# Kernel optimization log

Hardware: AMD Instinct MI355X
Metric: run time of the kernel (lower is better)

Reference implementation:

```python
import jax, jax.numpy as jnp
import numpy as np

B, H, W, C, NC = 4, 64, 64, 64, 19


def setup_inputs() -> dict:
    key = jax.random.key(0)
    ks = jax.random.split(key, 12)
    s = 0.05  # small init so sigmoid scores are not saturated
    return {
        "feature": jax.random.normal(ks[0], (B, H, W, C), dtype=jnp.float32),
        "predict": jax.random.normal(ks[1], (B, H, W, NC), dtype=jnp.float32),
        # height attention params (dim = H); k_linear in source is unused (q reused as k)
        "hq_w": jax.random.normal(ks[2], (H, H), dtype=jnp.float32) * s,
        "hq_b": jnp.zeros((H,), dtype=jnp.float32),
        "hv_w": jax.random.normal(ks[3], (H, H), dtype=jnp.float32) * s,
        "hv_b": jnp.zeros((H,), dtype=jnp.float32),
        # width attention params (dim = W)
        "wq_w": jax.random.normal(ks[4], (W, W), dtype=jnp.float32) * s,
        "wq_b": jnp.zeros((W,), dtype=jnp.float32),
        "wv_w": jax.random.normal(ks[5], (W, W), dtype=jnp.float32) * s,
        "wv_b": jnp.zeros((W,), dtype=jnp.float32),
        # gating scalars (nn.Parameter(torch.zeros(1)) in source; random here to exercise path)
        "h_gate": jax.random.normal(ks[6], (1,), dtype=jnp.float32) * 0.5,
        "w_gate": jax.random.normal(ks[7], (1,), dtype=jnp.float32) * 0.5,
        # 1x1 conv num_classes -> 1 (stored as [NC, 1] matrix; 1x1 conv == per-pixel linear)
        "conv_w": jax.random.normal(ks[8], (NC, 1), dtype=jnp.float32) * s,
        "conv_b": jnp.zeros((1,), dtype=jnp.float32),
    }


def _self_atten(x, wq, bq, wv, bv, dim):
    # Source uses q_linear for BOTH q and k (k_linear dead), softmax replaced by sigmoid.
    q = x @ wq + bq                                   # [B, N, dim]
    v = x @ wv + bv                                   # [B, N, dim]
    scores = jax.nn.sigmoid(jnp.einsum('bnd,bmd->bnm', q, q) / jnp.sqrt(jnp.float32(dim)))
    return jnp.einsum('bnm,bmd->bnd', scores, v)      # [B, N, dim]


def _axial(x, hq_w, hq_b, hv_w, hv_b, wq_w, wq_b, wv_w, wv_b, h_gate, w_gate):
    b, h, w, c = x.shape
    # height attention: seq = W*C, feature dim = H
    xh = x.transpose(0, 2, 3, 1).reshape(b, w * c, h)
    xh = _self_atten(xh, hq_w, hq_b, hv_w, hv_b, h)
    xh = xh.reshape(b, w, c, h).transpose(0, 3, 1, 2)  # back to [B,H,W,C]
    x = xh * h_gate + x
    # width attention: seq = H*C, feature dim = W
    xw = x.transpose(0, 1, 3, 2).reshape(b, h * c, w)
    xw = _self_atten(xw, wq_w, wq_b, wv_w, wv_b, w)
    xw = xw.reshape(b, h, c, w).transpose(0, 1, 3, 2)  # back to [B,H,W,C]
    x = xw * w_gate + x
    return x


def reference(feature, predict, hq_w, hq_b, hv_w, hv_b, wq_w, wq_b, wv_w, wv_b,
              h_gate, w_gate, conv_w, conv_b):
    feat = feature + _axial(feature, hq_w, hq_b, hv_w, hv_b,
                            wq_w, wq_b, wv_w, wv_b, h_gate, w_gate)
    p = 1.0 - jax.nn.sigmoid(predict)                 # [B,H,W,NC]
    p = p @ conv_w + conv_b                           # 1x1 conv -> [B,H,W,1]
    return p * feat                                   # broadcast gate -> [B,H,W,C]
```

## Files before the change

### kernel.cpp

```cpp
#include <hip/hip_runtime.h>

typedef _Float16 f16x8 __attribute__((ext_vector_type(8)));
typedef __fp16   fp16x2 __attribute__((ext_vector_type(2)));
typedef float f32x16 __attribute__((ext_vector_type(16)));

__device__ __forceinline__ unsigned pkrtz(float a, float b) {
    fp16x2 h = __builtin_amdgcn_cvt_pkrtz(a, b);
    union { fp16x2 h; unsigned u; } c; c.h = h; return c.u;
}

__device__ __forceinline__ unsigned short f2h(float f) {
    _Float16 h = (_Float16)f;
    union { _Float16 h; unsigned short s; } c; c.h = h; return c.s;
}

__global__ __launch_bounds__(256) void prep_kernel(
    const float* __restrict__ src,
    const float* __restrict__ wq, const float* __restrict__ bq,
    const float* __restrict__ wv, const float* __restrict__ bv,
    unsigned short* __restrict__ Qg, unsigned short* __restrict__ Vtg)
{
    __shared__ float slab[64][65];
    __shared__ float wqs[4096];
    __shared__ float wvs[4096];

    const int t  = threadIdx.x;
    const int bx = blockIdx.x, b = blockIdx.y;

    {
        const float4* wq4 = (const float4*)wq;
        const float4* wv4 = (const float4*)wv;
        float4* q4 = (float4*)wqs; float4* v4 = (float4*)wvs;
        #pragma unroll
        for (int i = 0; i < 4; ++i) {
            q4[i*256 + t] = wq4[i*256 + t];
            v4[i*256 + t] = wv4[i*256 + t];
        }
    }
    {
        const int k = t >> 2, c0 = (t & 3) << 4;
        const size_t sb = (size_t)b*262144 + (size_t)k*4096 + (size_t)bx*64 + c0;
        #pragma unroll
        for (int i = 0; i < 4; ++i)
            *(float4*)&slab[k][c0 + i*4] = *(const float4*)&src[sb + i*4];
    }
    __syncthreads();

    const int c = t & 63, jg = t >> 6;
    float qa[16], va[16];
    #pragma unroll
    for (int jj = 0; jj < 16; ++jj) { qa[jj] = bq[jg*16+jj]; va[jj] = bv[jg*16+jj]; }
    for (int k = 0; k < 64; ++k) {
        const float xv = slab[k][c];
        const float* wqr = &wqs[k*64 + jg*16];
        const float* wvr = &wvs[k*64 + jg*16];
        #pragma unroll
        for (int jj = 0; jj < 16; ++jj) {
            qa[jj] += xv * wqr[jj];
            va[jj] += xv * wvr[jj];
        }
    }
    const int token = bx*64 + c;
    union { unsigned u[8]; uint4 v[2]; } qp;
    #pragma unroll
    for (int jj = 0; jj < 8; ++jj) qp.u[jj] = pkrtz(qa[2*jj], qa[2*jj+1]);
    const size_t qoff = ((size_t)b*4096 + token)*64 + jg*16;
    *(uint4*)&Qg[qoff]     = qp.v[0];
    *(uint4*)&Qg[qoff + 8] = qp.v[1];
    #pragma unroll
    for (int jj = 0; jj < 16; ++jj)
        Vtg[((size_t)b*64 + jg*16 + jj)*4096 + token] = f2h(va[jj]);
}

__global__ __launch_bounds__(256) void prep_w_kernel(
    const float* __restrict__ feature, const float* __restrict__ Pin,
    const float* __restrict__ gate,
    const float* __restrict__ wq, const float* __restrict__ bq,
    const float* __restrict__ wv, const float* __restrict__ bv,
    unsigned short* __restrict__ Qg, unsigned short* __restrict__ Vtg,
    float* __restrict__ x1out, int nsplit)
{
    __shared__ float slab[64][65];
    __shared__ float wqs[4096];
    __shared__ float wvs[4096];

    const int t  = threadIdx.x;
    const int bx = blockIdx.x, b = blockIdx.y;

    {
        const float4* wq4 = (const float4*)wq;
        const float4* wv4 = (const float4*)wv;
        float4* q4 = (float4*)wqs; float4* v4 = (float4*)wvs;
        #pragma unroll
        for (int i = 0; i < 4; ++i) {
            q4[i*256 + t] = wq4[i*256 + t];
            v4[i*256 + t] = wv4[i*256 + t];
        }
    }
    {
        const int k = t >> 2, c0 = (t & 3) << 4;
        const size_t off = (size_t)bx*4096 + (size_t)k*64 + c0;
        const size_t fb  = (size_t)b*262144 + off;
        const float g = gate[0];
        #pragma unroll
        for (int i = 0; i < 4; ++i) {
            float4 v  = *(const float4*)&feature[fb + i*4];
            float sx = 0.f, sy = 0.f, sz = 0.f, sw = 0.f;
            for (int ks = 0; ks < nsplit; ++ks) {
                float4 pk = *(const float4*)&Pin[((size_t)(ks*4 + b) << 18) + off + i*4];
                sx += pk.x; sy += pk.y; sz += pk.z; sw += pk.w;
            }
            v.x += g * sx; v.y += g * sy; v.z += g * sz; v.w += g * sw;
            *(float4*)&slab[k][c0 + i*4] = v;
            *(float4*)&x1out[fb + i*4] = v;
        }
    }
    __syncthreads();

    const int c = t & 63, jg = t >> 6;
    float qa[16], va[16];
    #pragma unroll
    for (int jj = 0; jj < 16; ++jj) { qa[jj] = bq[jg*16+jj]; va[jj] = bv[jg*16+jj]; }
    for (int k = 0; k < 64; ++k) {
        const float xv = slab[k][c];
        const float* wqr = &wqs[k*64 + jg*16];
        const float* wvr = &wvs[k*64 + jg*16];
        #pragma unroll
        for (int jj = 0; jj < 16; ++jj) {
            qa[jj] += xv * wqr[jj];
            va[jj] += xv * wvr[jj];
        }
    }
    const int token = bx*64 + c;
    union { unsigned u[8]; uint4 v[2]; } qp;
    #pragma unroll
    for (int jj = 0; jj < 8; ++jj) qp.u[jj] = pkrtz(qa[2*jj], qa[2*jj+1]);
    const size_t qoff = ((size_t)b*4096 + token)*64 + jg*16;
    *(uint4*)&Qg[qoff]     = qp.v[0];
    *(uint4*)&Qg[qoff + 8] = qp.v[1];
    #pragma unroll
    for (int jj = 0; jj < 16; ++jj)
        Vtg[((size_t)b*64 + jg*16 + jj)*4096 + token] = f2h(va[jj]);
}

__global__ __launch_bounds__(256) void attn_kernel(
    const unsigned short* __restrict__ Qg,
    const unsigned short* __restrict__ Vtg,
    float* __restrict__ P)
{
    __shared__ unsigned short Ksh[2][64][72];
    __shared__ unsigned short Vts[2][64][72];

    const int t = threadIdx.x;
    const int mb = blockIdx.x, b = blockIdx.y, ksplit = blockIdx.z;
    const int nsp = gridDim.z;
    const int niter = 64 / nsp;
    const int keybase = ksplit * (4096 / nsp);
    const int lane = t & 63, w = t >> 6;
    const int l32 = lane & 31, hi = lane >> 5;

    const unsigned short* Qbase = Qg  + (size_t)b*262144;
    const unsigned short* Vbase = Vtg + (size_t)b*262144;

    f16x8 qb[4];
    {
        const unsigned short* qrow = Qbase + (size_t)(mb*128 + w*32 + l32)*64 + hi*8;
        const _Float16 sc = (_Float16)(-0.180336880f);
        #pragma unroll
        for (int s = 0; s < 4; ++s) {
            f16x8 q = *(const f16x8*)(qrow + s*16);
            qb[s] = q * sc;
        }
    }

    f32x16 y[2];
    #pragma unroll
    for (int i = 0; i < 16; ++i) { y[0][i] = 0.f; y[1][i] = 0.f; }

    const int lrow = t >> 2;
    const int loff = (t & 3) << 4;
    {
        const uint4* gk = (const uint4*)(Qbase + (size_t)(keybase + lrow)*64 + loff);
        uint4 k0 = gk[0], k1 = gk[1];
        const uint4* gv = (const uint4*)(Vbase + (size_t)lrow*4096 + keybase + loff);
        uint4 v0 = gv[0], v1 = gv[1];
        *(uint4*)&Ksh[0][lrow][loff]     = k0;
        *(uint4*)&Ksh[0][lrow][loff + 8] = k1;
        uint4 pa = { v0.x, v0.y, v1.x, v1.y };
        uint4 pb = { v0.z, v0.w, v1.z, v1.w };
        *(uint4*)&Vts[0][lrow][loff]     = pa;
        *(uint4*)&Vts[0][lrow][loff + 8] = pb;
    }
    __syncthreads();

    for (int kb = 0; kb < niter; ++kb) {
        const int cur = kb & 1, nxt = cur ^ 1;

        uint4 nk0 = {0,0,0,0}, nk1 = {0,0,0,0}, nv0 = {0,0,0,0}, nv1 = {0,0,0,0};
        if (kb < niter - 1) {
            const int keyn = keybase + (kb + 1)*64;
            const uint4* gk = (const uint4*)(Qbase + (size_t)(keyn + lrow)*64 + loff);
            nk0 = gk[0]; nk1 = gk[1];
            const uint4* gv = (const uint4*)(Vbase + (size_t)lrow*4096 + keyn + loff);
            nv0 = gv[0]; nv1 = gv[1];
        }

        f32x16 tt[2];
        #pragma unroll
        for (int i = 0; i < 16; ++i) { tt[0][i] = 0.f; tt[1][i] = 0.f; }
        #pragma unroll
        for (int s = 0; s < 4; ++s) {
            const int co = s*16 + hi*8;
            f16x8 ka0 = *(const f16x8*)&Ksh[cur][l32][co];
            f16x8 ka1 = *(const f16x8*)&Ksh[cur][32 + l32][co];
            tt[0] = __builtin_amdgcn_mfma_f32_32x32x16_f16(ka0, qb[s], tt[0], 0,0,0);
            tt[1] = __builtin_amdgcn_mfma_f32_32x32x16_f16(ka1, qb[s], tt[1], 0,0,0);
        }

        #pragma unroll
        for (int u = 0; u < 2; ++u) {
            unsigned pk_[8];
            #pragma unroll
            for (int pr = 0; pr < 8; ++pr) {
                float t0 = __builtin_fminf(tt[u][2*pr+0], 60.0f);
                float t1 = __builtin_fminf(tt[u][2*pr+1], 60.0f);
                float e0 = __builtin_exp2f(t0);
                float e1 = __builtin_exp2f(t1);
                float d0 = 1.0f + e0, d1 = 1.0f + e1;
                float rr = __builtin_amdgcn_rcpf(d0 * d1);
                pk_[pr] = pkrtz(rr * d1, rr * d0);
            }
            #pragma unroll
            for (int sp = 0; sp < 2; ++sp) {
                union { unsigned u4[4]; f16x8 v; } sa;
                sa.u4[0] = pk_[sp*4 + 0];
                sa.u4[1] = pk_[sp*4 + 1];
                sa.u4[2] = pk_[sp*4 + 2];
                sa.u4[3] = pk_[sp*4 + 3];
                const int ks = u*2 + sp;
                const int co = ks*16 + hi*8;
                f16x8 vb0 = *(const f16x8*)&Vts[cur][l32][co];
                f16x8 vb1 = *(const f16x8*)&Vts[cur][32 + l32][co];
                y[0] = __builtin_amdgcn_mfma_f32_32x32x16_f16(sa.v, vb0, y[0], 0,0,0);
                y[1] = __builtin_amdgcn_mfma_f32_32x32x16_f16(sa.v, vb1, y[1], 0,0,0);
            }
        }

        if (kb < niter - 1) {
            *(uint4*)&Ksh[nxt][lrow][loff]     = nk0;
            *(uint4*)&Ksh[nxt][lrow][loff + 8] = nk1;
            uint4 pa = { nv0.x, nv0.y, nv1.x, nv1.y };
            uint4 pb = { nv0.z, nv0.w, nv1.z, nv1.w };
            *(uint4*)&Vts[nxt][lrow][loff]     = pa;
            *(uint4*)&Vts[nxt][lrow][loff + 8] = pb;
        }
        __syncthreads();
    }

    float* Pp = P + (((size_t)(ksplit*4 + b)) << 18);
    const int token0 = mb*128 + w*32 + hi*4;
    #pragma unroll
    for (int dt = 0; dt < 2; ++dt) {
        const int d = dt*32 + l32;
        #pragma unroll
        for (int g = 0; g < 4; ++g) {
            float4 v;
            v.x = y[dt][4*g+0]; v.y = y[dt][4*g+1];
            v.z = y[dt][4*g+2]; v.w = y[dt][4*g+3];
            *(float4*)&Pp[(size_t)d*4096 + token0 + 8*g] = v;
        }
    }
}

__global__ __launch_bounds__(256) void final_kernel(
    const float* __restrict__ feature, const float* __restrict__ x1,
    const float* __restrict__ Pin, const float* __restrict__ predict,
    const float* __restrict__ conv_w, const float* __restrict__ conv_b,
    const float* __restrict__ gate, float* __restrict__ out, int nsplit)
{
    const int i4 = blockIdx.x * 256 + threadIdx.x;
    const int j = i4 << 2;
    const int pix = j >> 6;
    const float* row = predict + (size_t)pix * 19;
    float pv = conv_b[0];
    #pragma unroll
    for (int i = 0; i < 19; ++i) {
        float sg = __builtin_amdgcn_rcpf(1.0f + __builtin_exp2f(-1.442695041f * row[i]));
        pv += (1.0f - sg) * conv_w[i];
    }

    const int b = j >> 18, h = (j >> 12) & 63, d = (j >> 6) & 63, c = j & 63;
    const size_t pif = ((size_t)(b*64 + d) << 12) + h*64 + c;
    float sx = 0.f, sy = 0.f, sz = 0.f, sw = 0.f;
    for (int ks = 0; ks < nsplit; ++ks) {
        float4 pk = *(const float4*)&Pin[((size_t)ks << 20) + pif];
        sx += pk.x; sy += pk.y; sz += pk.z; sw += pk.w;
    }
    const float g = gate[0];
    float4 f = ((const float4*)feature)[i4];
    float4 x = ((const float4*)x1)[i4];
    float4 o;
    o.x = pv * (f.x + x.x + g * sx);
    o.y = pv * (f.y + x.y + g * sy);
    o.z = pv * (f.z + x.z + g * sz);
    o.w = pv * (f.w + x.w + g * sw);
    ((float4*)out)[i4] = o;
}

extern "C" void kernel_launch(void* const* d_in, const int* in_sizes, int n_in,
                              void* d_out, int out_size, void* d_ws, size_t ws_size,
                              hipStream_t stream) {
    const float* feature = (const float*)d_in[0];
    const float* predict = (const float*)d_in[1];
    const float* hq_w = (const float*)d_in[2];
    const float* hq_b = (const float*)d_in[3];
    const float* hv_w = (const float*)d_in[4];
    const float* hv_b = (const float*)d_in[5];
    const float* wq_w = (const float*)d_in[6];
    const float* wq_b = (const float*)d_in[7];
    const float* wv_w = (const float*)d_in[8];
    const float* wv_b = (const float*)d_in[9];
    const float* h_gate = (const float*)d_in[10];
    const float* w_gate = (const float*)d_in[11];
    const float* conv_w = (const float*)d_in[12];
    const float* conv_b = (const float*)d_in[13];
    float* out = (float*)d_out;

    char* ws = (char*)d_ws;
    unsigned short* Qg  = (unsigned short*)(ws);
    unsigned short* Vtg = (unsigned short*)(ws + (2u << 20));
    float*          x1  = (float*)(ws + (4u << 20));
    float*          P   = (float*)(ws + (8u << 20));
    const int nsplit = 4;

    dim3 blk(256);
    prep_kernel<<<dim3(64, 4), blk, 0, stream>>>(feature, hq_w, hq_b, hv_w, hv_b,
                                                 Qg, Vtg);
    attn_kernel<<<dim3(32, 4, nsplit), blk, 0, stream>>>(Qg, Vtg, P);
    prep_w_kernel<<<dim3(64, 4), blk, 0, stream>>>(feature, P, h_gate,
                                                   wq_w, wq_b, wv_w, wv_b,
                                                   Qg, Vtg, x1, nsplit);
    attn_kernel<<<dim3(32, 4, nsplit), blk, 0, stream>>>(Qg, Vtg, P);
    final_kernel<<<dim3(1024), blk, 0, stream>>>(feature, x1, P, predict,
                                                 conv_w, conv_b, w_gate, out, nsplit);
}
```

Before: 189.4 us.

## Read projection weights via scalar loads, zero-init MFMA accumulators, raise key split

```diff
diff --git a/kernel.cpp b/kernel.cpp
--- a/kernel.cpp
+++ b/kernel.cpp
@@ -21,22 +21,10 @@
     unsigned short* __restrict__ Qg, unsigned short* __restrict__ Vtg)
 {
     __shared__ float slab[64][65];
-    __shared__ float wqs[4096];
-    __shared__ float wvs[4096];
 
     const int t  = threadIdx.x;
     const int bx = blockIdx.x, b = blockIdx.y;
 
-    {
-        const float4* wq4 = (const float4*)wq;
-        const float4* wv4 = (const float4*)wv;
-        float4* q4 = (float4*)wqs; float4* v4 = (float4*)wvs;
-        #pragma unroll
-        for (int i = 0; i < 4; ++i) {
-            q4[i*256 + t] = wq4[i*256 + t];
-            v4[i*256 + t] = wv4[i*256 + t];
-        }
-    }
     {
         const int k = t >> 2, c0 = (t & 3) << 4;
         const size_t sb = (size_t)b*262144 + (size_t)k*4096 + (size_t)bx*64 + c0;
@@ -46,18 +34,20 @@
     }
     __syncthreads();
 
-    const int c = t & 63, jg = t >> 6;
+    const int c = t & 63;
+    const int jg = __builtin_amdgcn_readfirstlane(t >> 6);
+    const float* __restrict__ wqr = wq + jg*16;
+    const float* __restrict__ wvr = wv + jg*16;
     float qa[16], va[16];
     #pragma unroll
     for (int jj = 0; jj < 16; ++jj) { qa[jj] = bq[jg*16+jj]; va[jj] = bv[jg*16+jj]; }
+    #pragma unroll 4
     for (int k = 0; k < 64; ++k) {
         const float xv = slab[k][c];
-        const float* wqr = &wqs[k*64 + jg*16];
-        const float* wvr = &wvs[k*64 + jg*16];
         #pragma unroll
         for (int jj = 0; jj < 16; ++jj) {
-            qa[jj] += xv * wqr[jj];
-            va[jj] += xv * wvr[jj];
+            qa[jj] += xv * wqr[k*64 + jj];
+            va[jj] += xv * wvr[k*64 + jj];
         }
     }
     const int token = bx*64 + c;
@@ -81,22 +71,10 @@
     float* __restrict__ x1out, int nsplit)
 {
     __shared__ float slab[64][65];
-    __shared__ float wqs[4096];
-    __shared__ float wvs[4096];
 
     const int t  = threadIdx.x;
     const int bx = blockIdx.x, b = blockIdx.y;
 
-    {
-        const float4* wq4 = (const float4*)wq;
-        const float4* wv4 = (const float4*)wv;
-        float4* q4 = (float4*)wqs; float4* v4 = (float4*)wvs;
-        #pragma unroll
-        for (int i = 0; i < 4; ++i) {
-            q4[i*256 + t] = wq4[i*256 + t];
-            v4[i*256 + t] = wv4[i*256 + t];
-        }
-    }
     {
         const int k = t >> 2, c0 = (t & 3) << 4;
         const size_t off = (size_t)bx*4096 + (size_t)k*64 + c0;
@@ -117,18 +95,20 @@
     }
     __syncthreads();
 
-    const int c = t & 63, jg = t >> 6;
+    const int c = t & 63;
+    const int jg = __builtin_amdgcn_readfirstlane(t >> 6);
+    const float* __restrict__ wqr = wq + jg*16;
+    const float* __restrict__ wvr = wv + jg*16;
     float qa[16], va[16];
     #pragma unroll
     for (int jj = 0; jj < 16; ++jj) { qa[jj] = bq[jg*16+jj]; va[jj] = bv[jg*16+jj]; }
+    #pragma unroll 4
     for (int k = 0; k < 64; ++k) {
         const float xv = slab[k][c];
-        const float* wqr = &wqs[k*64 + jg*16];
-        const float* wvr = &wvs[k*64 + jg*16];
         #pragma unroll
         for (int jj = 0; jj < 16; ++jj) {
-            qa[jj] += xv * wqr[jj];
-            va[jj] += xv * wvr[jj];
+            qa[jj] += xv * wqr[k*64 + jj];
+            va[jj] += xv * wvr[k*64 + jj];
         }
     }
     const int token = bx*64 + c;
@@ -173,9 +153,12 @@
         }
     }
 
+    f32x16 fz;
+    #pragma unroll
+    for (int i = 0; i < 16; ++i) fz[i] = 0.f;
+
     f32x16 y[2];
-    #pragma unroll
-    for (int i = 0; i < 16; ++i) { y[0][i] = 0.f; y[1][i] = 0.f; }
+    y[0] = fz; y[1] = fz;
 
     const int lrow = t >> 2;
     const int loff = (t & 3) << 4;
@@ -207,14 +190,17 @@
 
         f32x16 tt[2];
         #pragma unroll
-        for (int i = 0; i < 16; ++i) { tt[0][i] = 0.f; tt[1][i] = 0.f; }
-        #pragma unroll
         for (int s = 0; s < 4; ++s) {
             const int co = s*16 + hi*8;
             f16x8 ka0 = *(const f16x8*)&Ksh[cur][l32][co];
             f16x8 ka1 = *(const f16x8*)&Ksh[cur][32 + l32][co];
-            tt[0] = __builtin_amdgcn_mfma_f32_32x32x16_f16(ka0, qb[s], tt[0], 0,0,0);
-            tt[1] = __builtin_amdgcn_mfma_f32_32x32x16_f16(ka1, qb[s], tt[1], 0,0,0);
+            if (s == 0) {
+                tt[0] = __builtin_amdgcn_mfma_f32_32x32x16_f16(ka0, qb[0], fz, 0,0,0);
+                tt[1] = __builtin_amdgcn_mfma_f32_32x32x16_f16(ka1, qb[0], fz, 0,0,0);
+            } else {
+                tt[0] = __builtin_amdgcn_mfma_f32_32x32x16_f16(ka0, qb[s], tt[0], 0,0,0);
+                tt[1] = __builtin_amdgcn_mfma_f32_32x32x16_f16(ka1, qb[s], tt[1], 0,0,0);
+            }
         }
 
         #pragma unroll
@@ -331,7 +317,7 @@
     unsigned short* Vtg = (unsigned short*)(ws + (2u << 20));
     float*          x1  = (float*)(ws + (4u << 20));
     float*          P   = (float*)(ws + (8u << 20));
-    const int nsplit = 4;
+    const int nsplit = (ws_size >= ((size_t)40 << 20)) ? 8 : 4;
 
     dim3 blk(256);
     prep_kernel<<<dim3(64, 4), blk, 0, stream>>>(feature, hq_w, hq_b, hv_w, hv_b,
```

After: 214.2 us. 1.13x slower.
